# Kernel optimization log

Measured on AMD Instinct MI355X. Metric: run time of the kernel, lower is better.

## Reference

```python
import jax, jax.numpy as jnp
import numpy as np

N_HEAD = 16

def setup_inputs() -> dict:
    key = jax.random.key(0)
    k1, k2, k3 = jax.random.split(key, 3)
    C = 1024
    x = jax.random.normal(k1, (2, 2048, C), dtype=jnp.float32)
    W_attn = jax.random.normal(k2, (C, 3 * C), dtype=jnp.float32) * (C ** -0.5)
    b_attn = jnp.zeros((3 * C,), dtype=jnp.float32)
    W_proj = jax.random.normal(k3, (C, C), dtype=jnp.float32) * (C ** -0.5)
    b_proj = jnp.zeros((C,), dtype=jnp.float32)
    return {"x": x, "W_attn": W_attn, "b_attn": b_attn, "W_proj": W_proj, "b_proj": b_proj}

def reference(x, W_attn, b_attn, W_proj, b_proj):
    B, T, C = x.shape
    H = N_HEAD
    hd = C // H
    qkv = x @ W_attn + b_attn                      # [B,T,3C]
    q, k, v = jnp.split(qkv, 3, axis=-1)
    q = q.reshape(B, T, H, hd).transpose(0, 2, 1, 3)  # [B,H,T,hd]
    k = k.reshape(B, T, H, hd).transpose(0, 2, 1, 3)
    v = v.reshape(B, T, H, hd).transpose(0, 2, 1, 3)
    att = jnp.einsum('bhqd,bhkd->bhqk', q, k) * (1.0 / jnp.sqrt(jnp.float32(hd)))
    causal = jnp.tril(jnp.ones((T, T), dtype=bool))
    att = jnp.where(causal[None, None, :, :], att, jnp.float32(-jnp.inf))
    att = jax.nn.softmax(att, axis=-1)
    y = jnp.einsum('bhqk,bhkd->bhqd', att, v)       # [B,H,T,hd]
    y = y.transpose(0, 2, 1, 3).reshape(B, T, C)
    return y @ W_proj + b_proj
```

## Files before the change

kernel.cpp:

```cpp
#include <hip/hip_runtime.h>
#include <hip/hip_bf16.h>

typedef unsigned short u16;
using frag_ab = __attribute__((ext_vector_type(8))) short;
using f32x4   = __attribute__((ext_vector_type(4))) float;
using u16x4   = __attribute__((ext_vector_type(4))) unsigned short;
using u16x8   = __attribute__((ext_vector_type(8))) unsigned short;

#define N_CTX   2048
#define NBATCH  2
#define CDIM    1024
#define NH      16
#define HD      64

__device__ __forceinline__ u16 f2b(float f) {
  __hip_bfloat16 h = __float2bfloat16(f);
  return __builtin_bit_cast(u16, h);
}

__device__ __forceinline__ f32x4 mfma16(frag_ab a, frag_ab b, f32x4 c) {
  return __builtin_amdgcn_mfma_f32_16x16x32_bf16(a, b, c, 0, 0, 0);
}

#define GLDS16(src, dst) \
  __builtin_amdgcn_global_load_lds((const __attribute__((address_space(1))) void*)(src), \
                                   (__attribute__((address_space(3))) void*)(dst), 16, 0, 0)

__global__ __launch_bounds__(256) void prep_all(const float* __restrict__ x, u16* __restrict__ xb,
                                                const float* __restrict__ Wa, u16* __restrict__ Wab,
                                                const float* __restrict__ Wp, u16* __restrict__ Wpb) {
  __shared__ float tile[32][33];
  const int blk = blockIdx.x;
  if (blk < 2048) {
    int i = blk * 256 + threadIdx.x;
    const f32x4* ip = (const f32x4*)x;
    f32x4 a = ip[2 * i], b2 = ip[2 * i + 1];
    u16x8 r;
    #pragma unroll
    for (int j = 0; j < 4; ++j) { r[j] = f2b(a[j]); r[4 + j] = f2b(b2[j]); }
    ((u16x8*)xb)[i] = r;
    return;
  }
  const float* in; u16* out; int K, N, bx, by;
  if (blk < 5120) {
    int idx = blk - 2048; in = Wa; out = Wab; K = CDIM; N = 3 * CDIM;
    bx = idx % 96; by = idx / 96;
  } else {
    int idx = blk - 5120; in = Wp; out = Wpb; K = CDIM; N = CDIM;
    bx = idx & 31; by = idx >> 5;
  }
  int n0 = bx * 32, k0 = by * 32;
  int c = threadIdx.x & 31, r0 = threadIdx.x >> 5;
  #pragma unroll
  for (int i = 0; i < 4; ++i) {
    int r = r0 + i * 8;
    tile[r][c] = in[(size_t)(k0 + r) * N + n0 + c];
  }
  __syncthreads();
  int n = threadIdx.x >> 3, kq = threadIdx.x & 7;
  u16x4 pk;
  #pragma unroll
  for (int j = 0; j < 4; ++j) pk[j] = f2b(tile[kq * 4 + j][n]);
  *(u16x4*)&out[(size_t)(n0 + n) * K + k0 + kq * 4] = pk;
}

__global__ __launch_bounds__(512, 4) void gemm_qkv128(const u16* __restrict__ A,
                                                      const u16* __restrict__ Bt,
                                                      const float* __restrict__ bias,
                                                      u16* __restrict__ Qo, u16* __restrict__ Ko,
                                                      u16* __restrict__ Vto) {
  __shared__ __align__(16) u16 As[2][128 * 64];
  __shared__ __align__(16) u16 Bs[2][192 * 64];
  const int tid = threadIdx.x, w = tid >> 6, lane = tid & 63;
  const int g = lane >> 4, lr = lane & 15;
  const int wr = w >> 2, wc = w & 3;
  const int bid = blockIdx.x;
  const int swz = (bid & 7) * 64 + (bid >> 3);
  const int tm = (swz & 31) * 128, tn = (swz >> 5) * 192;

  f32x4 acc[4][3];
  #pragma unroll
  for (int mi = 0; mi < 4; ++mi)
    #pragma unroll
    for (int ni = 0; ni < 3; ++ni)
      acc[mi][ni] = (f32x4){0.f, 0.f, 0.f, 0.f};

  auto STAGE = [&](int d, int kt) {
    const int k0 = kt << 6;
    #pragma unroll
    for (int j = 0; j < 2; ++j) {
      int ci = j * 512 + tid, row = ci >> 3, c8 = ci & 7;
      GLDS16(A + (size_t)(tm + row) * CDIM + k0 + ((c8 ^ (row & 7)) << 3),
             &As[d][row * 64 + c8 * 8]);
    }
    #pragma unroll
    for (int j = 0; j < 3; ++j) {
      int ci = j * 512 + tid, row = ci >> 3, c8 = ci & 7;
      GLDS16(Bt + (size_t)(tn + row) * CDIM + k0 + ((c8 ^ (row & 7)) << 3),
             &Bs[d][row * 64 + c8 * 8]);
    }
  };

  STAGE(0, 0);
  asm volatile("s_waitcnt vmcnt(0)" ::: "memory");
  __builtin_amdgcn_s_barrier();

  const int x7 = lr & 7;
  for (int t = 0; t < 16; ++t) {
    const int cur = t & 1;
    if (t < 15) STAGE(cur ^ 1, t + 1);

    frag_ab af[4][2], bf[3][2];
    #pragma unroll
    for (int mi = 0; mi < 4; ++mi) {
      int row = wr * 64 + mi * 16 + lr;
      #pragma unroll
      for (int ks = 0; ks < 2; ++ks)
        af[mi][ks] = *(const frag_ab*)&As[cur][row * 64 + ((((ks << 2) | g) ^ x7) << 3)];
    }
    #pragma unroll
    for (int ni = 0; ni < 3; ++ni) {
      int row = wc * 48 + ni * 16 + lr;
      #pragma unroll
      for (int ks = 0; ks < 2; ++ks)
        bf[ni][ks] = *(const frag_ab*)&Bs[cur][row * 64 + ((((ks << 2) | g) ^ x7) << 3)];
    }
    __builtin_amdgcn_s_setprio(1);
    #pragma unroll
    for (int mi = 0; mi < 4; ++mi)
      #pragma unroll
      for (int ni = 0; ni < 3; ++ni)
        #pragma unroll
        for (int ks = 0; ks < 2; ++ks)
          acc[mi][ni] = mfma16(af[mi][ks], bf[ni][ks], acc[mi][ni]);
    __builtin_amdgcn_s_setprio(0);

    asm volatile("s_waitcnt vmcnt(0)" ::: "memory");
    __builtin_amdgcn_s_barrier();
  }

  #pragma unroll
  for (int ni = 0; ni < 3; ++ni) {
    int n = tn + wc * 48 + ni * 16 + lr;
    float bv = bias[n];
    int which = n >> 10, c = n & 1023, h = c >> 6, d = c & 63;
    #pragma unroll
    for (int mi = 0; mi < 4; ++mi) {
      if (which == 2) {
        int t0 = tm + wr * 64 + mi * 16 + g * 4;
        int bb = t0 >> 11, tt = t0 & (N_CTX - 1);
        u16x4 pk;
        #pragma unroll
        for (int r = 0; r < 4; ++r) pk[r] = f2b(acc[mi][ni][r] + bv);
        *(u16x4*)&Vto[((size_t)(bb * NH + h) * HD + d) * N_CTX + tt] = pk;
      } else {
        u16* dst = (which == 0) ? Qo : Ko;
        float scl = (which == 0) ? 0.180336881f : 1.0f;
        #pragma unroll
        for (int r = 0; r < 4; ++r) {
          int m = tm + wr * 64 + mi * 16 + g * 4 + r;
          int bb = m >> 11, tt = m & (N_CTX - 1);
          dst[((size_t)(bb * NH + h) * N_CTX + tt) * HD + d] = f2b((acc[mi][ni][r] + bv) * scl);
        }
      }
    }
  }
}

__global__ __launch_bounds__(512, 4) void gemm_proj128(const u16* __restrict__ A,
                                                       const u16* __restrict__ Bt,
                                                       const float* __restrict__ bias,
                                                       float* __restrict__ out) {
  __shared__ __align__(16) u16 As[3][128 * 64];
  __shared__ __align__(16) u16 Bs[3][64 * 64];
  const int tid = threadIdx.x, w = tid >> 6, lane = tid & 63;
  const int g = lane >> 4, lr = lane & 15;
  const int wr = w >> 1, wc = w & 1;
  const int bid = blockIdx.x;
  const int swz = (bid & 7) * 64 + (bid >> 3);
  const int tm = (swz & 31) * 128, tn = (swz >> 5) * 64;

  f32x4 acc[2][2];
  #pragma unroll
  for (int mi = 0; mi < 2; ++mi)
    #pragma unroll
    for (int ni = 0; ni < 2; ++ni)
      acc[mi][ni] = (f32x4){0.f, 0.f, 0.f, 0.f};

  auto STAGE = [&](int d, int kt) {
    const int k0 = kt << 6;
    #pragma unroll
    for (int j = 0; j < 2; ++j) {
      int ci = j * 512 + tid, row = ci >> 3, c8 = ci & 7;
      GLDS16(A + (size_t)(tm + row) * CDIM + k0 + ((c8 ^ (row & 7)) << 3),
             &As[d][row * 64 + c8 * 8]);
    }
    {
      int row = tid >> 3, c8 = tid & 7;
      GLDS16(Bt + (size_t)(tn + row) * CDIM + k0 + ((c8 ^ (row & 7)) << 3),
             &Bs[d][row * 64 + c8 * 8]);
    }
  };

  STAGE(0, 0);
  STAGE(1, 1);
  asm volatile("s_waitcnt vmcnt(3)" ::: "memory");
  __builtin_amdgcn_s_barrier();

  const int x7 = lr & 7;
  int cur = 0;
  for (int t = 0; t < 16; ++t) {
    if (t < 14) STAGE((cur + 2) % 3, t + 2);

    frag_ab af[2][2], bf[2][2];
    #pragma unroll
    for (int mi = 0; mi < 2; ++mi) {
      int row = wr * 32 + mi * 16 + lr;
      #pragma unroll
      for (int ks = 0; ks < 2; ++ks)
        af[mi][ks] = *(const frag_ab*)&As[cur][row * 64 + ((((ks << 2) | g) ^ x7) << 3)];
    }
    #pragma unroll
    for (int ni = 0; ni < 2; ++ni) {
      int row = wc * 32 + ni * 16 + lr;
      #pragma unroll
      for (int ks = 0; ks < 2; ++ks)
        bf[ni][ks] = *(const frag_ab*)&Bs[cur][row * 64 + ((((ks << 2) | g) ^ x7) << 3)];
    }
    __builtin_amdgcn_s_setprio(1);
    #pragma unroll
    for (int mi = 0; mi < 2; ++mi)
      #pragma unroll
      for (int ni = 0; ni < 2; ++ni)
        #pragma unroll
        for (int ks = 0; ks < 2; ++ks)
          acc[mi][ni] = mfma16(af[mi][ks], bf[ni][ks], acc[mi][ni]);
    __builtin_amdgcn_s_setprio(0);

    if (t < 14) { asm volatile("s_waitcnt vmcnt(3)" ::: "memory"); }
    else        { asm volatile("s_waitcnt vmcnt(0)" ::: "memory"); }
    __builtin_amdgcn_s_barrier();
    cur = (cur + 1) % 3;
  }

  #pragma unroll
  for (int ni = 0; ni < 2; ++ni) {
    int n = tn + wc * 32 + ni * 16 + lr;
    float bv = bias[n];
    #pragma unroll
    for (int mi = 0; mi < 2; ++mi)
      #pragma unroll
      for (int r = 0; r < 4; ++r) {
        int m = tm + wr * 32 + mi * 16 + g * 4 + r;
        out[(size_t)m * CDIM + n] = acc[mi][ni][r] + bv;
      }
  }
}

__global__ __launch_bounds__(512, 4) void attn_fwd(const u16* __restrict__ Q, const u16* __restrict__ K,
                                                   const u16* __restrict__ Vt, u16* __restrict__ Y) {
  __shared__ __align__(16) u16 Ks[4][64 * 64];
  __shared__ __align__(16) u16 Vs[4][64 * 64];
  const int orig = blockIdx.x;
  const int bh = (orig & 7) * 4 + ((orig >> 3) & 3);
  const int qt = 31 - (orig >> 5);
  const int tid = threadIdx.x, w = tid >> 6, lane = tid & 63;
  const int grp = w >> 2, wq = w & 3;
  const int g = lane >> 4, lr = lane & 15;
  const size_t base = (size_t)bh * N_CTX * HD;
  const u16* Kbh = K + base;
  const u16* Vbh = Vt + base;

  const int c8 = tid & 7, srow = tid >> 3;
  const size_t kOff = (size_t)srow * HD + (size_t)((c8 ^ (srow & 7)) * 8);
  const size_t vOff = (size_t)srow * N_CTX + (size_t)((c8 ^ (srow & 7)) * 8);

  frag_ab qf[2];
  {
    const u16* qp = Q + base + (size_t)(qt * 64 + wq * 16 + lr) * HD + g * 8;
    qf[0] = *(const frag_ab*)qp;  qf[1] = *(const frag_ab*)(qp + 32);
  }

  float ps = 0.f;
  f32x4 o[4];
  #pragma unroll
  for (int d = 0; d < 4; ++d) o[d] = (f32x4){0.f, 0.f, 0.f, 0.f};

  auto STAGE = [&](int b, int kt) {
    GLDS16(Kbh + (size_t)kt * 64 * HD + kOff, &Ks[b][(size_t)tid * 8]);
    GLDS16(Vbh + (size_t)kt * 64 + vOff,      &Vs[b][(size_t)tid * 8]);
  };

  const int niter = (qt + 2) >> 1;
  STAGE(0, 0);
  STAGE(1, 1);
  asm volatile("s_waitcnt vmcnt(0)" ::: "memory");
  __builtin_amdgcn_s_barrier();

  const int qrow = wq * 16 + lr;
  for (int i = 0; i < niter; ++i) {
    const int t0 = 2 * i;
    const int t  = t0 + grp;
    if (i + 1 < niter) { STAGE((t0 + 2) & 3, t0 + 2); STAGE((t0 + 3) & 3, t0 + 3); }

    if (t <= qt) {
      const int bb = t & 3;
      frag_ab kf[4][2];
      #pragma unroll
      for (int nf = 0; nf < 4; ++nf)
        #pragma unroll
        for (int ks = 0; ks < 2; ++ks)
          kf[nf][ks] = *(const frag_ab*)&Ks[bb][(size_t)(nf * 16 + lr) * 64 +
                                                (size_t)((((ks << 2) | g) ^ (lr & 7)) * 8)];
      f32x4 s[4];
      __builtin_amdgcn_s_setprio(1);
      #pragma unroll
      for (int j = 0; j < 4; ++j) {
        f32x4 a = (f32x4){0.f, 0.f, 0.f, 0.f};
        a = mfma16(kf[j][0], qf[0], a);
        a = mfma16(kf[j][1], qf[1], a);
        s[j] = a;
      }
      __builtin_amdgcn_s_setprio(0);
      if (t == qt) {
        #pragma unroll
        for (int nf = 0; nf < 4; ++nf)
          #pragma unroll
          for (int r = 0; r < 4; ++r)
            if (nf * 16 + g * 4 + r > qrow) s[nf][r] = -1e30f;
      }
      #pragma unroll
      for (int j = 0; j < 4; ++j)
        #pragma unroll
        for (int r = 0; r < 4; ++r)
          s[j][r] = __builtin_amdgcn_exp2f(s[j][r]);
      ps += ((s[0][0]+s[0][1])+(s[0][2]+s[0][3])) + ((s[1][0]+s[1][1])+(s[1][2]+s[1][3]))
          + ((s[2][0]+s[2][1])+(s[2][2]+s[2][3])) + ((s[3][0]+s[3][1])+(s[3][2]+s[3][3]));
      frag_ab pa[2];
      #pragma unroll
      for (int ks = 0; ks < 2; ++ks)
        #pragma unroll
        for (int j = 0; j < 4; ++j) {
          pa[ks][j]     = (short)f2b(s[2 * ks][j]);
          pa[ks][4 + j] = (short)f2b(s[2 * ks + 1][j]);
        }
      #pragma unroll
      for (int d = 0; d < 4; ++d) {
        const int row = (d * 16 + lr) * 64;
        frag_ab vf[2];
        #pragma unroll
        for (int ks = 0; ks < 2; ++ks) {
          u16x4 lo = *(const u16x4*)&Vs[bb][row + (((ks * 4 + (g >> 1)) ^ (lr & 7)) * 8) + (g & 1) * 4];
          u16x4 hi = *(const u16x4*)&Vs[bb][row + (((ks * 4 + 2 + (g >> 1)) ^ (lr & 7)) * 8) + (g & 1) * 4];
          #pragma unroll
          for (int j = 0; j < 4; ++j) { vf[ks][j] = (short)lo[j]; vf[ks][4 + j] = (short)hi[j]; }
        }
        __builtin_amdgcn_s_setprio(1);
        o[d] = mfma16(pa[0], vf[0], o[d]);
        o[d] = mfma16(pa[1], vf[1], o[d]);
        __builtin_amdgcn_s_setprio(0);
      }
    }

    asm volatile("s_waitcnt vmcnt(0)" ::: "memory");
    __builtin_amdgcn_s_barrier();
  }

  ps += __shfl_xor(ps, 16, 64);
  ps += __shfl_xor(ps, 32, 64);

  float* SO = (float*)&Ks[0][0];
  float* PS = (float*)&Vs[0][0];

  if (grp == 1) {
    #pragma unroll
    for (int d = 0; d < 4; ++d)
      #pragma unroll
      for (int r = 0; r < 4; ++r)
        SO[(wq * 16 + g * 4 + r) * 64 + d * 16 + lr] = o[d][r];
    if (g == 0) PS[wq * 16 + lr] = ps;
  }
  __syncthreads();

  if (grp == 0) {
    const int b = bh >> 4, h = bh & 15;
    float li = 1.0f / (ps + PS[wq * 16 + lr]);
    #pragma unroll
    for (int r = 0; r < 4; ++r) {
      int src = (lane & 48) | (((lane >> 4) & 3) * 4 + r);
      float lir = __shfl(li, src, 64);
      int row = qt * 64 + wq * 16 + g * 4 + r;
      #pragma unroll
      for (int d = 0; d < 4; ++d) {
        float val = (o[d][r] + SO[(wq * 16 + g * 4 + r) * 64 + d * 16 + lr]) * lir;
        Y[((size_t)(b * N_CTX + row)) * CDIM + h * HD + d * 16 + lr] = f2b(val);
      }
    }
  }
}

extern "C" void kernel_launch(void* const* d_in, const int* in_sizes, int n_in,
                              void* d_out, int out_size, void* d_ws, size_t ws_size,
                              hipStream_t stream) {
  const float* x      = (const float*)d_in[0];
  const float* W_attn = (const float*)d_in[1];
  const float* b_attn = (const float*)d_in[2];
  const float* W_proj = (const float*)d_in[3];
  const float* b_proj = (const float*)d_in[4];
  float* out = (float*)d_out;
  char* ws = (char*)d_ws;

  u16* xb  = (u16*)(ws);
  u16* Wab = (u16*)(ws + ((size_t)8 << 20));
  u16* Wpb = (u16*)(ws + ((size_t)14 << 20));
  u16* Qb  = (u16*)(ws + ((size_t)16 << 20));
  u16* Kb  = (u16*)(ws + ((size_t)24 << 20));
  u16* Vtb = (u16*)(ws + ((size_t)32 << 20));
  u16* yb  = xb;

  prep_all<<<6144, 256, 0, stream>>>(x, xb, W_attn, Wab, W_proj, Wpb);
  gemm_qkv128<<<512, 512, 0, stream>>>(xb, Wab, b_attn, Qb, Kb, Vtb);
  attn_fwd<<<1024, 512, 0, stream>>>(Qb, Kb, Vtb, yb);
  gemm_proj128<<<512, 512, 0, stream>>>(yb, Wpb, b_proj, out);
}
```

Measured before the change: 89.67 us.

## Pair early and late 128-row query tiles per attention block to balance causal work

The attention kernel now gives each block two 128-row query tiles, one from the start and one from the end of the sequence, so every block does roughly equal causal work. Each K/V tile staged in shared memory is reused across four query fragments per wave instead of one, which cuts K/V global and LDS traffic per unit of work. The grid shrinks from 1024 to 256 blocks and the occupancy hint drops to 2, trading fewer resident waves and more registers for better reuse and load balance. The max-free exp2 softmax from before is kept.

```diff
diff --git a/kernel.cpp b/kernel.cpp
--- a/kernel.cpp
+++ b/kernel.cpp
@@ -257,107 +257,130 @@
   }
 }
 
-__global__ __launch_bounds__(512, 4) void attn_fwd(const u16* __restrict__ Q, const u16* __restrict__ K,
+__global__ __launch_bounds__(512, 2) void attn_fwd(const u16* __restrict__ Q, const u16* __restrict__ K,
                                                    const u16* __restrict__ Vt, u16* __restrict__ Y) {
-  __shared__ __align__(16) u16 Ks[4][64 * 64];
-  __shared__ __align__(16) u16 Vs[4][64 * 64];
+  __shared__ __align__(16) u16 KV[8][64 * 64];
+  __shared__ float PSb[256];
   const int orig = blockIdx.x;
   const int bh = (orig & 7) * 4 + ((orig >> 3) & 3);
-  const int qt = 31 - (orig >> 5);
-  const int tid = threadIdx.x, w = tid >> 6, lane = tid & 63;
-  const int grp = w >> 2, wq = w & 3;
+  const int p  = orig >> 5;
+  const int RA = 128 * p, RB = 2048 - 128 * (p + 1);
+  const int tid = threadIdx.x, w8 = tid >> 6, lane = tid & 63;
+  const int grp = w8 >> 2, w = w8 & 3;
   const int g = lane >> 4, lr = lane & 15;
   const size_t base = (size_t)bh * N_CTX * HD;
   const u16* Kbh = K + base;
   const u16* Vbh = Vt + base;
 
-  const int c8 = tid & 7, srow = tid >> 3;
+  const int c8 = tid & 7, srow = (tid >> 3) & 63;
   const size_t kOff = (size_t)srow * HD + (size_t)((c8 ^ (srow & 7)) * 8);
   const size_t vOff = (size_t)srow * N_CTX + (size_t)((c8 ^ (srow & 7)) * 8);
 
-  frag_ab qf[2];
+  frag_ab qA0[2], qA1[2], qB0[2], qB1[2];
   {
-    const u16* qp = Q + base + (size_t)(qt * 64 + wq * 16 + lr) * HD + g * 8;
-    qf[0] = *(const frag_ab*)qp;  qf[1] = *(const frag_ab*)(qp + 32);
-  }
-
-  float ps = 0.f;
-  f32x4 o[4];
-  #pragma unroll
-  for (int d = 0; d < 4; ++d) o[d] = (f32x4){0.f, 0.f, 0.f, 0.f};
+    const u16* q0 = Q + base + (size_t)(RA + w * 32 + lr) * HD + g * 8;
+    qA0[0] = *(const frag_ab*)q0;  qA0[1] = *(const frag_ab*)(q0 + 32);
+    const u16* q1 = Q + base + (size_t)(RA + w * 32 + 16 + lr) * HD + g * 8;
+    qA1[0] = *(const frag_ab*)q1;  qA1[1] = *(const frag_ab*)(q1 + 32);
+    const u16* q2 = Q + base + (size_t)(RB + w * 32 + lr) * HD + g * 8;
+    qB0[0] = *(const frag_ab*)q2;  qB0[1] = *(const frag_ab*)(q2 + 32);
+    const u16* q3 = Q + base + (size_t)(RB + w * 32 + 16 + lr) * HD + g * 8;
+    qB1[0] = *(const frag_ab*)q3;  qB1[1] = *(const frag_ab*)(q3 + 32);
+  }
+  const int off0 = (w * 32) & 63, off1 = (w * 32 + 16) & 63;
+  const int TA0 = (RA + w * 32) >> 6, TA1 = (RA + w * 32 + 16) >> 6;
+  const int TB0 = (RB + w * 32) >> 6, TB1 = (RB + w * 32 + 16) >> 6;
+
+  f32x4 oA0[4], oA1[4], oB0[4], oB1[4];
+  float pA0 = 0.f, pA1 = 0.f, pB0 = 0.f, pB1 = 0.f;
+  #pragma unroll
+  for (int d = 0; d < 4; ++d) {
+    oA0[d] = (f32x4){0,0,0,0};  oA1[d] = (f32x4){0,0,0,0};
+    oB0[d] = (f32x4){0,0,0,0};  oB1[d] = (f32x4){0,0,0,0};
+  }
 
   auto STAGE = [&](int b, int kt) {
-    GLDS16(Kbh + (size_t)kt * 64 * HD + kOff, &Ks[b][(size_t)tid * 8]);
-    GLDS16(Vbh + (size_t)kt * 64 + vOff,      &Vs[b][(size_t)tid * 8]);
+    GLDS16(Kbh + (size_t)kt * 64 * HD + kOff, &KV[b][(size_t)tid * 8]);
+    GLDS16(Vbh + (size_t)kt * 64 + vOff,      &KV[4 + b][(size_t)tid * 8]);
   };
 
-  const int niter = (qt + 2) >> 1;
+  frag_ab kf[4][2];
+  auto qk = [&](const frag_ab (&qf)[2], frag_ab (&pa)[2], float& ps, bool diag, int off) {
+    f32x4 s[4];
+    __builtin_amdgcn_s_setprio(1);
+    #pragma unroll
+    for (int j = 0; j < 4; ++j) {
+      f32x4 a = (f32x4){0.f, 0.f, 0.f, 0.f};
+      a = mfma16(kf[j][0], qf[0], a);
+      a = mfma16(kf[j][1], qf[1], a);
+      s[j] = a;
+    }
+    __builtin_amdgcn_s_setprio(0);
+    if (diag) {
+      #pragma unroll
+      for (int nf = 0; nf < 4; ++nf)
+        #pragma unroll
+        for (int r = 0; r < 4; ++r)
+          if (nf * 16 + g * 4 + r > off + lr) s[nf][r] = -1e30f;
+    }
+    #pragma unroll
+    for (int j = 0; j < 4; ++j)
+      #pragma unroll
+      for (int r = 0; r < 4; ++r)
+        s[j][r] = __builtin_amdgcn_exp2f(s[j][r]);
+    ps += ((s[0][0]+s[0][1])+(s[0][2]+s[0][3])) + ((s[1][0]+s[1][1])+(s[1][2]+s[1][3]))
+        + ((s[2][0]+s[2][1])+(s[2][2]+s[2][3])) + ((s[3][0]+s[3][1])+(s[3][2]+s[3][3]));
+    #pragma unroll
+    for (int ks = 0; ks < 2; ++ks)
+      #pragma unroll
+      for (int j = 0; j < 4; ++j) {
+        pa[ks][j]     = (short)f2b(s[2 * ks][j]);
+        pa[ks][4 + j] = (short)f2b(s[2 * ks + 1][j]);
+      }
+  };
+
+  const int niter = 16 - p;
   STAGE(0, 0);
   STAGE(1, 1);
   asm volatile("s_waitcnt vmcnt(0)" ::: "memory");
   __builtin_amdgcn_s_barrier();
 
-  const int qrow = wq * 16 + lr;
   for (int i = 0; i < niter; ++i) {
-    const int t0 = 2 * i;
-    const int t  = t0 + grp;
-    if (i + 1 < niter) { STAGE((t0 + 2) & 3, t0 + 2); STAGE((t0 + 3) & 3, t0 + 3); }
-
-    if (t <= qt) {
+    const int t = 2 * i + grp;
+    if (i + 1 < niter) { STAGE((2 * i + 2) & 3, 2 * i + 2); STAGE((2 * i + 3) & 3, 2 * i + 3); }
+
+    const bool aB0 = t <= TB0, aB1 = t <= TB1;
+    const bool aA0 = t <= TA0, aA1 = t <= TA1;
+    if (aB0 | aB1) {
       const int bb = t & 3;
-      frag_ab kf[4][2];
       #pragma unroll
       for (int nf = 0; nf < 4; ++nf)
         #pragma unroll
         for (int ks = 0; ks < 2; ++ks)
-          kf[nf][ks] = *(const frag_ab*)&Ks[bb][(size_t)(nf * 16 + lr) * 64 +
+          kf[nf][ks] = *(const frag_ab*)&KV[bb][(size_t)(nf * 16 + lr) * 64 +
                                                 (size_t)((((ks << 2) | g) ^ (lr & 7)) * 8)];
-      f32x4 s[4];
-      __builtin_amdgcn_s_setprio(1);
-      #pragma unroll
-      for (int j = 0; j < 4; ++j) {
-        f32x4 a = (f32x4){0.f, 0.f, 0.f, 0.f};
-        a = mfma16(kf[j][0], qf[0], a);
-        a = mfma16(kf[j][1], qf[1], a);
-        s[j] = a;
-      }
-      __builtin_amdgcn_s_setprio(0);
-      if (t == qt) {
-        #pragma unroll
-        for (int nf = 0; nf < 4; ++nf)
-          #pragma unroll
-          for (int r = 0; r < 4; ++r)
-            if (nf * 16 + g * 4 + r > qrow) s[nf][r] = -1e30f;
-      }
-      #pragma unroll
-      for (int j = 0; j < 4; ++j)
-        #pragma unroll
-        for (int r = 0; r < 4; ++r)
-          s[j][r] = __builtin_amdgcn_exp2f(s[j][r]);
-      ps += ((s[0][0]+s[0][1])+(s[0][2]+s[0][3])) + ((s[1][0]+s[1][1])+(s[1][2]+s[1][3]))
-          + ((s[2][0]+s[2][1])+(s[2][2]+s[2][3])) + ((s[3][0]+s[3][1])+(s[3][2]+s[3][3]));
-      frag_ab pa[2];
-      #pragma unroll
-      for (int ks = 0; ks < 2; ++ks)
-        #pragma unroll
-        for (int j = 0; j < 4; ++j) {
-          pa[ks][j]     = (short)f2b(s[2 * ks][j]);
-          pa[ks][4 + j] = (short)f2b(s[2 * ks + 1][j]);
-        }
+      frag_ab paA0[2], paA1[2], paB0[2], paB1[2];
+      if (aB0) qk(qB0, paB0, pB0, t == TB0, off0);
+      if (aB1) qk(qB1, paB1, pB1, t == TB1, off1);
+      if (aA0) qk(qA0, paA0, pA0, t == TA0, off0);
+      if (aA1) qk(qA1, paA1, pA1, t == TA1, off1);
+
       #pragma unroll
       for (int d = 0; d < 4; ++d) {
         const int row = (d * 16 + lr) * 64;
         frag_ab vf[2];
         #pragma unroll
         for (int ks = 0; ks < 2; ++ks) {
-          u16x4 lo = *(const u16x4*)&Vs[bb][row + (((ks * 4 + (g >> 1)) ^ (lr & 7)) * 8) + (g & 1) * 4];
-          u16x4 hi = *(const u16x4*)&Vs[bb][row + (((ks * 4 + 2 + (g >> 1)) ^ (lr & 7)) * 8) + (g & 1) * 4];
+          u16x4 lo = *(const u16x4*)&KV[4 + bb][row + (((ks * 4 + (g >> 1)) ^ (lr & 7)) * 8) + (g & 1) * 4];
+          u16x4 hi = *(const u16x4*)&KV[4 + bb][row + (((ks * 4 + 2 + (g >> 1)) ^ (lr & 7)) * 8) + (g & 1) * 4];
           #pragma unroll
           for (int j = 0; j < 4; ++j) { vf[ks][j] = (short)lo[j]; vf[ks][4 + j] = (short)hi[j]; }
         }
         __builtin_amdgcn_s_setprio(1);
-        o[d] = mfma16(pa[0], vf[0], o[d]);
-        o[d] = mfma16(pa[1], vf[1], o[d]);
+        if (aB0) { oB0[d] = mfma16(paB0[0], vf[0], oB0[d]); oB0[d] = mfma16(paB0[1], vf[1], oB0[d]); }
+        if (aB1) { oB1[d] = mfma16(paB1[0], vf[0], oB1[d]); oB1[d] = mfma16(paB1[1], vf[1], oB1[d]); }
+        if (aA0) { oA0[d] = mfma16(paA0[0], vf[0], oA0[d]); oA0[d] = mfma16(paA0[1], vf[1], oA0[d]); }
+        if (aA1) { oA1[d] = mfma16(paA1[0], vf[0], oA1[d]); oA1[d] = mfma16(paA1[1], vf[1], oA1[d]); }
         __builtin_amdgcn_s_setprio(0);
       }
     }
@@ -366,34 +389,56 @@
     __builtin_amdgcn_s_barrier();
   }
 
-  ps += __shfl_xor(ps, 16, 64);
-  ps += __shfl_xor(ps, 32, 64);
-
-  float* SO = (float*)&Ks[0][0];
-  float* PS = (float*)&Vs[0][0];
+  pA0 += __shfl_xor(pA0, 16, 64);  pA0 += __shfl_xor(pA0, 32, 64);
+  pA1 += __shfl_xor(pA1, 16, 64);  pA1 += __shfl_xor(pA1, 32, 64);
+  pB0 += __shfl_xor(pB0, 16, 64);  pB0 += __shfl_xor(pB0, 32, 64);
+  pB1 += __shfl_xor(pB1, 16, 64);  pB1 += __shfl_xor(pB1, 32, 64);
+
+  float* SO = (float*)&KV[0][0];
 
   if (grp == 1) {
     #pragma unroll
     for (int d = 0; d < 4; ++d)
       #pragma unroll
-      for (int r = 0; r < 4; ++r)
-        SO[(wq * 16 + g * 4 + r) * 64 + d * 16 + lr] = o[d][r];
-    if (g == 0) PS[wq * 16 + lr] = ps;
+      for (int r = 0; r < 4; ++r) {
+        SO[(w * 32 + g * 4 + r) * 64 + d * 16 + lr]            = oA0[d][r];
+        SO[(w * 32 + 16 + g * 4 + r) * 64 + d * 16 + lr]       = oA1[d][r];
+        SO[(128 + w * 32 + g * 4 + r) * 64 + d * 16 + lr]      = oB0[d][r];
+        SO[(128 + w * 32 + 16 + g * 4 + r) * 64 + d * 16 + lr] = oB1[d][r];
+      }
+    if (g == 0) {
+      PSb[w * 32 + lr]            = pA0;
+      PSb[w * 32 + 16 + lr]       = pA1;
+      PSb[128 + w * 32 + lr]      = pB0;
+      PSb[128 + w * 32 + 16 + lr] = pB1;
+    }
   }
   __syncthreads();
 
   if (grp == 0) {
     const int b = bh >> 4, h = bh & 15;
-    float li = 1.0f / (ps + PS[wq * 16 + lr]);
+    float liA0 = 1.0f / (pA0 + PSb[w * 32 + lr]);
+    float liA1 = 1.0f / (pA1 + PSb[w * 32 + 16 + lr]);
+    float liB0 = 1.0f / (pB0 + PSb[128 + w * 32 + lr]);
+    float liB1 = 1.0f / (pB1 + PSb[128 + w * 32 + 16 + lr]);
     #pragma unroll
     for (int r = 0; r < 4; ++r) {
       int src = (lane & 48) | (((lane >> 4) & 3) * 4 + r);
-      float lir = __shfl(li, src, 64);
-      int row = qt * 64 + wq * 16 + g * 4 + r;
+      float lA0 = __shfl(liA0, src, 64), lA1 = __shfl(liA1, src, 64);
+      float lB0 = __shfl(liB0, src, 64), lB1 = __shfl(liB1, src, 64);
+      int rA0 = RA + w * 32 + g * 4 + r,      rA1 = RA + w * 32 + 16 + g * 4 + r;
+      int rB0 = RB + w * 32 + g * 4 + r,      rB1 = RB + w * 32 + 16 + g * 4 + r;
       #pragma unroll
       for (int d = 0; d < 4; ++d) {
-        float val = (o[d][r] + SO[(wq * 16 + g * 4 + r) * 64 + d * 16 + lr]) * lir;
-        Y[((size_t)(b * N_CTX + row)) * CDIM + h * HD + d * 16 + lr] = f2b(val);
+        int col = h * HD + d * 16 + lr;
+        float vA0 = (oA0[d][r] + SO[(w * 32 + g * 4 + r) * 64 + d * 16 + lr]) * lA0;
+        float vA1 = (oA1[d][r] + SO[(w * 32 + 16 + g * 4 + r) * 64 + d * 16 + lr]) * lA1;
+        float vB0 = (oB0[d][r] + SO[(128 + w * 32 + g * 4 + r) * 64 + d * 16 + lr]) * lB0;
+        float vB1 = (oB1[d][r] + SO[(128 + w * 32 + 16 + g * 4 + r) * 64 + d * 16 + lr]) * lB1;
+        Y[((size_t)(b * N_CTX + rA0)) * CDIM + col] = f2b(vA0);
+        Y[((size_t)(b * N_CTX + rA1)) * CDIM + col] = f2b(vA1);
+        Y[((size_t)(b * N_CTX + rB0)) * CDIM + col] = f2b(vB0);
+        Y[((size_t)(b * N_CTX + rB1)) * CDIM + col] = f2b(vB1);
       }
     }
   }
@@ -420,6 +465,6 @@
 
   prep_all<<<6144, 256, 0, stream>>>(x, xb, W_attn, Wab, W_proj, Wpb);
   gemm_qkv128<<<512, 512, 0, stream>>>(xb, Wab, b_attn, Qb, Kb, Vtb);
-  attn_fwd<<<1024, 512, 0, stream>>>(Qb, Kb, Vtb, yb);
+  attn_fwd<<<256, 512, 0, stream>>>(Qb, Kb, Vtb, yb);
   gemm_proj128<<<512, 512, 0, stream>>>(yb, Wpb, b_proj, out);
 }
```

Measured after the change: 94.92 us. 5.9% more time.
